# Kernel optimization log

Measured on AMD Instinct MI355X. Metric: run time of the kernel, lower is better.

Reference implementation:

```python
import jax, jax.numpy as jnp
import numpy as np

B = 65536          # batch of response rows
R = 262144         # number of response rows
N_CELLS = 900
N_MISSING = 100
N_DRUGS = 256
NFEAT = 1024
CELL_EMB = 1024
DRUG_EMB = 128
HID = 200
NDOSES = 9


def setup_inputs() -> dict:
    key = jax.random.key(0)
    ks = jax.random.split(key, 16)
    inp = {
        "idx": jax.random.randint(ks[0], (B,), 0, R, dtype=jnp.int32),
        "tidx": jax.random.randint(ks[1], (B,), 0, R, dtype=jnp.int32),
        "is_missing": jax.random.randint(ks[2], (R,), 0, 2, dtype=jnp.int32),
        "cell_map": jax.random.randint(ks[3], (R,), 0, N_MISSING, dtype=jnp.int32),
        "drug_map": jax.random.randint(ks[4], (R,), 0, N_DRUGS, dtype=jnp.int32),
        "cell_features": jax.random.normal(ks[5], (N_CELLS, NFEAT), jnp.float32),
        "missing_emb": jax.random.normal(ks[6], (N_MISSING, CELL_EMB), jnp.float32) * 0.02,
        "drug_emb": jax.random.normal(ks[7], (N_DRUGS, DRUG_EMB), jnp.float32) * 0.02,
        "W1": jax.random.normal(ks[8], (NFEAT, CELL_EMB), jnp.float32) * 0.02,
        "b1": jax.random.normal(ks[9], (CELL_EMB,), jnp.float32) * 0.02,
        "Wf1": jax.random.normal(ks[10], (CELL_EMB + DRUG_EMB, HID), jnp.float32) * 0.02,
        "bf1": jax.random.normal(ks[11], (HID,), jnp.float32) * 0.02,
        "Wf2": jax.random.normal(ks[12], (HID, HID), jnp.float32) * 0.02,
        "bf2": jax.random.normal(ks[13], (HID,), jnp.float32) * 0.02,
        "Wf3": jax.random.normal(ks[14], (HID, NDOSES), jnp.float32) * 0.02,
        "bf3": jax.random.normal(ks[15], (NDOSES,), jnp.float32) * 0.02,
    }
    return inp


def _l2_normalize(x, eps=1e-12):
    # torch F.normalize: x / max(||x||_2, eps)
    n = jnp.sqrt(jnp.sum(x * x, axis=1, keepdims=True))
    return x / jnp.maximum(n, eps)


def reference(idx, tidx, is_missing, cell_map, drug_map, cell_features,
              missing_emb, drug_emb, W1, b1, Wf1, bf1, Wf2, bf2, Wf3, bf3):
    # --- cell_lookup, vectorized (eval mode: dropout = identity) ---
    cm = cell_map[idx]                                   # [B]
    miss = (is_missing[idx] != 0)[:, None]               # [B,1] bool
    feat = cell_features[cm]                             # [B, NFEAT]
    present = jax.nn.relu(feat @ W1 + b1)                # [B, CELL_EMB]
    missing = missing_emb[cm]                            # [B, CELL_EMB]
    cell_embeds = jnp.where(miss, missing, present)
    # --- drug_lookup ---
    drug_embeds = drug_emb[drug_map[tidx]]               # [B, DRUG_EMB]
    # --- embeds_to_predictions ---
    cell_embeds = _l2_normalize(cell_embeds)
    drug_embeds = _l2_normalize(drug_embeds)
    x = jnp.concatenate([cell_embeds, drug_embeds], axis=1)
    h = jax.nn.relu(x @ Wf1 + bf1)
    h = jax.nn.relu(h @ Wf2 + bf2)
    fwd = h @ Wf3 + bf3                                  # [B, NDOSES]
    base = fwd[:, 0:1]
    mu = jnp.concatenate(
        [base, base + jnp.cumsum(jax.nn.softplus(fwd[:, 1:]), axis=1)], axis=1)
    return mu  # [B, NDOSES + ... ] -> actually [B, 1 + (NDOSES-1) + 1]? No: [B, NDOSES]? see note
```

## Files before the change

kernel.cpp:

```cpp
#include <hip/hip_runtime.h>
#include <hip/hip_bf16.h>

#define NFEAT 1024
#define CELL_EMB 1024
#define DRUG_EMB 128
#define HID 200
#define NDOSES 9
#define N_MISSING 100
#define N_DRUGS 256
#define S 16
#define MUSTRIDE 12

typedef __hip_bfloat16 bf16;
typedef __attribute__((ext_vector_type(8))) short short8;
typedef __attribute__((ext_vector_type(4))) short short4v;
typedef __attribute__((ext_vector_type(4))) float float4v;

__device__ __forceinline__ float bf2f(short s) {
    unsigned u = ((unsigned)(unsigned short)s) << 16;
    return __builtin_bit_cast(float, u);
}
__device__ __forceinline__ short f2bf(float f) {
    unsigned u = __builtin_bit_cast(unsigned, f);
    unsigned r = (u + 0x7FFFu + ((u >> 16) & 1u)) >> 16;
    return (short)r;
}
template <bool F32>
__device__ __forceinline__ float ld(const void* p, int i) {
    if (F32) return ((const float*)p)[i];
    return bf2f(((const short*)p)[i]);
}
__device__ __forceinline__ float ldr(const void* p, int i, bool f32) {
    return f32 ? ((const float*)p)[i] : bf2f(((const short*)p)[i]);
}
__device__ __forceinline__ float softplusf(float x) {
    return (x > 20.f) ? x : log1pf(expf(x));
}

__device__ __forceinline__ bool sniff_f32(const unsigned short* __restrict__ w1) {
    int lane = threadIdx.x & 63;
    unsigned short h = w1[lane];
    bool hit = ((lane & 1) == 0) && (((h >> 7) & 0xFFu) >= 130u);
    return __ballot(hit) != 0ull;
}


#define GP_PRESENT 800
#define GP_DC_END (GP_PRESENT + 256)
#define GP_PB_END (GP_DC_END + 25)
#define GP_CZ_END (GP_PB_END + 40)

__global__ __launch_bounds__(256) void mega_prep_k(const void* __restrict__ CF,
                                                   const unsigned short* __restrict__ W1u,
                                                   const void* __restrict__ b1,
                                                   const void* __restrict__ drug_emb,
                                                   const void* __restrict__ Wf1,
                                                   const void* __restrict__ Wf2,
                                                   float* __restrict__ P8,
                                                   float* __restrict__ Dc,
                                                   short8* __restrict__ Bf,
                                                   float* __restrict__ Cc) {
    bool f32 = sniff_f32(W1u);
    const void* W1 = (const void*)W1u;
    int blk = blockIdx.x, tid = threadIdx.x;

    if (blk < GP_PRESENT) {
        __shared__ float feat[128];
        int c = blk >> 3, kc = blk & 7;
        if (tid < 128) feat[tid] = ldr(CF, c * NFEAT + kc * 128 + tid, f32);
        __syncthreads();
        int j0 = tid * 4;
        float a0 = 0.f, a1 = 0.f, a2 = 0.f, a3 = 0.f;
        if (f32) {
            const float* w = (const float*)W1 + (size_t)(kc * 128) * CELL_EMB + j0;
#pragma unroll 8
            for (int k = 0; k < 128; ++k) {
                float4v wv = *(const float4v*)(w + (size_t)k * CELL_EMB);
                float fk = feat[k];
                a0 = fmaf(fk, wv[0], a0); a1 = fmaf(fk, wv[1], a1);
                a2 = fmaf(fk, wv[2], a2); a3 = fmaf(fk, wv[3], a3);
            }
        } else {
            const short* w = (const short*)W1 + (size_t)(kc * 128) * CELL_EMB + j0;
#pragma unroll 8
            for (int k = 0; k < 128; ++k) {
                short4v wv = *(const short4v*)(w + (size_t)k * CELL_EMB);
                float fk = feat[k];
                a0 = fmaf(fk, bf2f(wv[0]), a0); a1 = fmaf(fk, bf2f(wv[1]), a1);
                a2 = fmaf(fk, bf2f(wv[2]), a2); a3 = fmaf(fk, bf2f(wv[3]), a3);
            }
        }
        if (kc == 0) {
            a0 += ldr(b1, j0 + 0, f32); a1 += ldr(b1, j0 + 1, f32);
            a2 += ldr(b1, j0 + 2, f32); a3 += ldr(b1, j0 + 3, f32);
        }
        float4v o; o[0] = a0; o[1] = a1; o[2] = a2; o[3] = a3;
        *(float4v*)(P8 + ((size_t)(kc * N_MISSING + c)) * CELL_EMB + j0) = o;
    } else if (blk < GP_DC_END) {
        __shared__ float x[DRUG_EMB];
        __shared__ float red[4];
        int d = blk - GP_PRESENT;
        if (tid < DRUG_EMB) x[tid] = ldr(drug_emb, d * DRUG_EMB + tid, f32);
        __syncthreads();
        float ss = 0.f;
        if (tid < DRUG_EMB) ss = x[tid] * x[tid];
        for (int o = 32; o > 0; o >>= 1) ss += __shfl_down(ss, o, 64);
        if ((tid & 63) == 0) red[tid >> 6] = ss;
        __syncthreads();
        float inv = 1.f / fmaxf(sqrtf(red[0] + red[1] + red[2] + red[3]), 1e-12f);
        if (tid < HID) {
            float acc = 0.f;
#pragma unroll 8
            for (int k = 0; k < DRUG_EMB; ++k)
                acc = fmaf(x[k], ldr(Wf1, (CELL_EMB + k) * HID + tid, f32), acc);
            Dc[d * HID + tid] = acc * inv;
        }
    } else if (blk < GP_PB_END) {
        int t = (blk - GP_DC_END) * 256 + tid;
        if (t < 6272) {
            int l = t & 63, chunk = t >> 6;
            int p = chunk / 49, rem = chunk - p * 49;
            int nt = rem / 7, s = rem - nt * 7;
            int n = p * 112 + nt * 16 + (l & 15);
            int k0 = s * 32 + (l >> 4) * 8;
            short8 v;
#pragma unroll
            for (int j = 0; j < 8; ++j) {
                int k = k0 + j;
                v[j] = (k < HID && n < HID) ? f2bf(ldr(Wf2, k * HID + n, f32)) : (short)0;
            }
            Bf[t] = v;
        }
    } else {
        int i = (blk - GP_PB_END) * 1024 + tid * 4;
        if (i < 200 * HID) {
            float4v z; z[0] = 0.f; z[1] = 0.f; z[2] = 0.f; z[3] = 0.f;
            *(float4v*)(Cc + i) = z;
        }
    }
}

__global__ __launch_bounds__(256) void cc_k(const unsigned short* __restrict__ W1u,
                                            const float* __restrict__ P8,
                                            const void* __restrict__ missing_emb,
                                            const void* __restrict__ Wf1,
                                            float* __restrict__ Cc) {
    __shared__ __align__(16) float x[128];
    __shared__ float red[4];
    bool f32 = sniff_f32(W1u);
    int r = blockIdx.x, kc = blockIdx.y, tid = threadIdx.x;
    int e0 = tid * 4;
    float4v v;
    if (r < N_MISSING) {
        v[0] = 0.f; v[1] = 0.f; v[2] = 0.f; v[3] = 0.f;
#pragma unroll
        for (int p = 0; p < 8; ++p) {
            float4v t = *(const float4v*)(P8 + ((size_t)(p * N_MISSING + r)) * CELL_EMB + e0);
            v[0] += t[0]; v[1] += t[1]; v[2] += t[2]; v[3] += t[3];
        }
        v[0] = fmaxf(v[0], 0.f); v[1] = fmaxf(v[1], 0.f);
        v[2] = fmaxf(v[2], 0.f); v[3] = fmaxf(v[3], 0.f);
    } else if (f32) {
        v = *(const float4v*)((const float*)missing_emb + (size_t)(r - N_MISSING) * CELL_EMB + e0);
    } else {
        short4v s = *(const short4v*)((const short*)missing_emb + (size_t)(r - N_MISSING) * CELL_EMB + e0);
        v[0] = bf2f(s[0]); v[1] = bf2f(s[1]); v[2] = bf2f(s[2]); v[3] = bf2f(s[3]);
    }
    if ((tid >> 5) == kc) *(float4v*)(x + (e0 - kc * 128)) = v;
    float ss = v[0] * v[0] + v[1] * v[1] + v[2] * v[2] + v[3] * v[3];
    for (int o = 32; o > 0; o >>= 1) ss += __shfl_down(ss, o, 64);
    if ((tid & 63) == 0) red[tid >> 6] = ss;
    __syncthreads();
    float inv = 1.f / fmaxf(sqrtf(red[0] + red[1] + red[2] + red[3]), 1e-12f);
    if (tid < HID) {
        float acc = 0.f;
        if (f32) {
            const float* w = (const float*)Wf1 + (size_t)(kc * 128) * HID + tid;
#pragma unroll 8
            for (int k = 0; k < 128; ++k)
                acc = fmaf(x[k], w[(size_t)k * HID], acc);
        } else {
            const short* w = (const short*)Wf1 + (size_t)(kc * 128) * HID + tid;
#pragma unroll 8
            for (int k = 0; k < 128; ++k)
                acc = fmaf(x[k], bf2f(w[(size_t)k * HID]), acc);
        }
        atomicAdd(&Cc[r * HID + tid], acc * inv);
    }
}

#define KSTEPS 7
#define NTP 7
#define KP 224
#define MB 64

__global__ __launch_bounds__(256) void pair_k(const unsigned short* __restrict__ W1u,
                                              const float* __restrict__ Cc,
                                              const float* __restrict__ Dc,
                                              const void* __restrict__ bf1,
                                              const void* __restrict__ bf2,
                                              const void* __restrict__ Wf3,
                                              const short8* __restrict__ Bf,
                                              float* __restrict__ mu) {
    __shared__ float Crow[KP];
    __shared__ float bf2s[KP];
    __shared__ short wf3s[KP * NDOSES];
    bool f32 = sniff_f32(W1u);
    int tid = threadIdx.x;
    int lane = tid & 63, w = tid >> 6;
    int q = lane >> 4, col = lane & 15;
    int r0 = blockIdx.x * MB;
    int c = r0 >> 8;
    int d0 = r0 & 255;

    for (int k = tid; k < KP; k += 256) {
        Crow[k] = (k < HID) ? Cc[c * HID + k] + ldr(bf1, k, f32) : 0.f;
        bf2s[k] = (k < HID) ? ldr(bf2, k, f32) : 0.f;
    }
    for (int t = tid; t < KP * NDOSES; t += 256) {
        int k = t / NDOSES, dd = t - k * NDOSES;
        wf3s[t] = (k < HID) ? f2bf(ldr(Wf3, k * NDOSES + dd, f32)) : (short)0;
    }
    __syncthreads();

    int arow = d0 + w * 16 + col;

    short8 a[KSTEPS];
#pragma unroll
    for (int s = 0; s < KSTEPS; ++s) {
        int k0 = s * 32 + q * 8;
        if (k0 < HID) {
            float4v c0 = *(const float4v*)(&Crow[k0]);
            float4v c1 = *(const float4v*)(&Crow[k0 + 4]);
            float4v dv0 = *(const float4v*)(Dc + (size_t)arow * HID + k0);
            float4v dv1 = *(const float4v*)(Dc + (size_t)arow * HID + k0 + 4);
#pragma unroll
            for (int j = 0; j < 4; ++j) {
                a[s][j]     = f2bf(fmaxf(c0[j] + dv0[j], 0.f));
                a[s][j + 4] = f2bf(fmaxf(c1[j] + dv1[j], 0.f));
            }
        } else {
#pragma unroll
            for (int j = 0; j < 8; ++j) a[s][j] = 0;
        }
    }

    float fw[4][9];
#pragma unroll
    for (int i = 0; i < 4; ++i)
#pragma unroll
        for (int dd = 0; dd < 9; ++dd) fw[i][dd] = 0.f;

    for (int p = 0; p < 2; ++p) {
        float4v acc[NTP];
#pragma unroll
        for (int nt = 0; nt < NTP; ++nt) acc[nt] = 0.f;
#pragma unroll
        for (int s = 0; s < KSTEPS; ++s) {
#pragma unroll
            for (int nt = 0; nt < NTP; ++nt) {
                short8 bb = Bf[(size_t)((p * 7 + nt) * 7 + s) * 64 + lane];
                acc[nt] = __builtin_amdgcn_mfma_f32_16x16x32_bf16(a[s], bb, acc[nt], 0, 0, 0);
            }
        }
#pragma unroll
        for (int nt = 0; nt < NTP; ++nt) {
            int n = p * 112 + nt * 16 + col;
            float bb2 = bf2s[n];
            float w3[9];
#pragma unroll
            for (int dd = 0; dd < 9; ++dd) w3[dd] = bf2f(wf3s[n * NDOSES + dd]);
#pragma unroll
            for (int rg = 0; rg < 4; ++rg) {
                float h2 = fmaxf(acc[nt][rg] + bb2, 0.f);
#pragma unroll
                for (int dd = 0; dd < 9; ++dd)
                    fw[rg][dd] = fmaf(h2, w3[dd], fw[rg][dd]);
            }
        }
    }
#pragma unroll
    for (int i = 0; i < 4; ++i)
#pragma unroll
        for (int dd = 0; dd < 9; ++dd) {
            float v = fw[i][dd];
            v += __shfl_xor(v, 1, 16);
            v += __shfl_xor(v, 2, 16);
            v += __shfl_xor(v, 4, 16);
            v += __shfl_xor(v, 8, 16);
            fw[i][dd] = v;
        }
#pragma unroll
    for (int i = 0; i < 4; ++i) {
        int row = r0 + w * 16 + q * 4 + i;
        float myval = 0.f;
#pragma unroll
        for (int dd = 0; dd < 9; ++dd) myval = (col == dd) ? fw[i][dd] : myval;
        float v = (col == 0) ? myval : softplusf(myval);
        float t1 = __shfl_up(v, 1, 16); if (col >= 1) v += t1;
        float t2 = __shfl_up(v, 2, 16); if (col >= 2) v += t2;
        float t4 = __shfl_up(v, 4, 16); if (col >= 4) v += t4;
        float t8 = __shfl_up(v, 8, 16); if (col >= 8) v += t8;
        if (col < NDOSES) mu[(size_t)row * MUSTRIDE + col] = v;
    }
}

__global__ __launch_bounds__(256) void gather_k(const unsigned short* __restrict__ W1u,
                                                const int* __restrict__ idx,
                                                const int* __restrict__ tidx,
                                                const int* __restrict__ is_missing,
                                                const int* __restrict__ cell_map,
                                                const int* __restrict__ drug_map,
                                                const float* __restrict__ mu,
                                                void* __restrict__ out, int nB) {
    bool f32 = sniff_f32(W1u);
    int b = blockIdx.x * 256 + threadIdx.x;
    if (b >= nB) return;
    int i = idx[b];
    int cm = cell_map[i];
    int kc = (is_missing[i] != 0) ? (N_MISSING + cm) : cm;
    int kd = drug_map[tidx[b]];
    const float* mr = mu + (size_t)(kc * 256 + kd) * MUSTRIDE;
    float4v m0 = *(const float4v*)mr;
    float4v m1 = *(const float4v*)(mr + 4);
    float m8 = mr[8];
    float vals[9] = {m0[0], m0[1], m0[2], m0[3], m1[0], m1[1], m1[2], m1[3], m8};
    if (f32) {
        float* o = (float*)out + (size_t)b * NDOSES;
#pragma unroll
        for (int dd = 0; dd < 9; ++dd) o[dd] = vals[dd];
    } else {
        short* o = (short*)out + (size_t)b * NDOSES;
#pragma unroll
        for (int dd = 0; dd < 9; ++dd) o[dd] = f2bf(vals[dd]);
    }
}


__global__ void sniff_kernel(const unsigned short* __restrict__ w1bits, int* __restrict__ flag) {
    if (threadIdx.x == 0 && blockIdx.x == 0) {
        int f = 0;
        for (int i = 0; i < 512; ++i) {
            unsigned int e = (w1bits[i] >> 7) & 0xFFu;
            if (e >= 130u) f = 1;
        }
        *flag = f;
    }
}

template <bool F32>
__global__ __launch_bounds__(256) void present_kernel(const int* __restrict__ flag,
                                                      const void* __restrict__ cell_features,
                                                      const void* __restrict__ W1,
                                                      const void* __restrict__ b1,
                                                      float* __restrict__ P) {
    if (*flag != (int)F32) return;
    __shared__ float feat[NFEAT];
    int c = blockIdx.x, jb = blockIdx.y;
    for (int k = threadIdx.x; k < NFEAT; k += 256)
        feat[k] = ld<F32>(cell_features, c * NFEAT + k);
    __syncthreads();
    int j = jb * 256 + threadIdx.x;
    float acc = ld<F32>(b1, j);
    for (int k = 0; k < NFEAT; ++k)
        acc = fmaf(feat[k], ld<F32>(W1, k * CELL_EMB + j), acc);
    P[c * CELL_EMB + j] = fmaxf(acc, 0.f);
}

template <bool F32>
__global__ __launch_bounds__(256) void cc_kernel(const int* __restrict__ flag,
                                                 const float* __restrict__ P,
                                                 const void* __restrict__ missing_emb,
                                                 const void* __restrict__ Wf1,
                                                 float* __restrict__ Cc) {
    if (*flag != (int)F32) return;
    int r = blockIdx.x;
    __shared__ float x[CELL_EMB];
    __shared__ float red[4];
    if (r < N_MISSING) {
        for (int k = threadIdx.x; k < CELL_EMB; k += 256) x[k] = P[r * CELL_EMB + k];
    } else {
        for (int k = threadIdx.x; k < CELL_EMB; k += 256)
            x[k] = ld<F32>(missing_emb, (r - N_MISSING) * CELL_EMB + k);
    }
    __syncthreads();
    float ss = 0.f;
    for (int k = threadIdx.x; k < CELL_EMB; k += 256) ss += x[k] * x[k];
    for (int o = 32; o > 0; o >>= 1) ss += __shfl_down(ss, o, 64);
    if ((threadIdx.x & 63) == 0) red[threadIdx.x >> 6] = ss;
    __syncthreads();
    float inv = 1.f / fmaxf(sqrtf(red[0] + red[1] + red[2] + red[3]), 1e-12f);
    int j = threadIdx.x;
    if (j < HID) {
        float acc = 0.f;
        for (int k = 0; k < CELL_EMB; ++k)
            acc = fmaf(x[k], ld<F32>(Wf1, k * HID + j), acc);
        Cc[r * HID + j] = acc * inv;
    }
}

template <bool F32>
__global__ __launch_bounds__(256) void dc_kernel(const int* __restrict__ flag,
                                                 const void* __restrict__ drug_emb,
                                                 const void* __restrict__ Wf1,
                                                 float* __restrict__ Dc) {
    if (*flag != (int)F32) return;
    int d = blockIdx.x;
    __shared__ float x[DRUG_EMB];
    __shared__ float red[4];
    if (threadIdx.x < DRUG_EMB) x[threadIdx.x] = ld<F32>(drug_emb, d * DRUG_EMB + threadIdx.x);
    __syncthreads();
    float ss = 0.f;
    if (threadIdx.x < DRUG_EMB) ss = x[threadIdx.x] * x[threadIdx.x];
    for (int o = 32; o > 0; o >>= 1) ss += __shfl_down(ss, o, 64);
    if ((threadIdx.x & 63) == 0) red[threadIdx.x >> 6] = ss;
    __syncthreads();
    float inv = 1.f / fmaxf(sqrtf(red[0] + red[1] + red[2] + red[3]), 1e-12f);
    int j = threadIdx.x;
    if (j < HID) {
        float acc = 0.f;
        for (int k = 0; k < DRUG_EMB; ++k)
            acc = fmaf(x[k], ld<F32>(Wf1, (CELL_EMB + k) * HID + j), acc);
        Dc[d * HID + j] = acc * inv;
    }
}

template <bool F32>
__global__ __launch_bounds__(256) void main_kernel(const int* __restrict__ flag,
                                                   const int* __restrict__ idx,
                                                   const int* __restrict__ tidx,
                                                   const int* __restrict__ is_missing,
                                                   const int* __restrict__ cell_map,
                                                   const int* __restrict__ drug_map,
                                                   const float* __restrict__ Cc,
                                                   const float* __restrict__ Dc,
                                                   const void* __restrict__ bf1,
                                                   const void* __restrict__ Wf2,
                                                   const void* __restrict__ bf2,
                                                   const void* __restrict__ Wf3,
                                                   const void* __restrict__ bf3,
                                                   void* __restrict__ out, int nB) {
    if (*flag != (int)F32) return;
    __shared__ float h1t[HID][S];
    __shared__ float h2[S][HID];
    __shared__ float wf3s[HID * NDOSES];
    __shared__ float bf3s[NDOSES];
    __shared__ int keyc[S], keyd[S];
    __shared__ float fwds[S][NDOSES];

    int b0 = blockIdx.x * S;
    int tid = threadIdx.x;

    if (tid < S) {
        int b = b0 + tid;
        if (b < nB) {
            int i = idx[b];
            int cm = cell_map[i];
            keyc[tid] = (is_missing[i] != 0) ? (N_MISSING + cm) : cm;
            keyd[tid] = drug_map[tidx[b]];
        } else { keyc[tid] = 0; keyd[tid] = 0; }
    }
    for (int t = tid; t < HID * NDOSES; t += 256) wf3s[t] = ld<F32>(Wf3, t);
    if (tid < NDOSES) bf3s[tid] = ld<F32>(bf3, tid);
    __syncthreads();

    for (int t = tid; t < S * HID; t += 256) {
        int s = t / HID;
        int j = t - s * HID;
        float v = Cc[keyc[s] * HID + j] + Dc[keyd[s] * HID + j] + ld<F32>(bf1, j);
        h1t[j][s] = fmaxf(v, 0.f);
    }
    __syncthreads();

    if (tid < HID) {
        float acc[S];
#pragma unroll
        for (int s = 0; s < S; ++s) acc[s] = 0.f;
        for (int i = 0; i < HID; ++i) {
            float wv = ld<F32>(Wf2, i * HID + tid);
#pragma unroll
            for (int s = 0; s < S; ++s) acc[s] = fmaf(h1t[i][s], wv, acc[s]);
        }
        float bb = ld<F32>(bf2, tid);
#pragma unroll
        for (int s = 0; s < S; ++s) h2[s][tid] = fmaxf(acc[s] + bb, 0.f);
    }
    __syncthreads();

    if (tid < S * NDOSES) {
        int s = tid / NDOSES;
        int k = tid - s * NDOSES;
        float acc = bf3s[k];
        for (int j = 0; j < HID; ++j)
            acc = fmaf(h2[s][j], wf3s[j * NDOSES + k], acc);
        fwds[s][k] = acc;
    }
    __syncthreads();

    if (tid < S && b0 + tid < nB) {
        float m = fwds[tid][0];
        long o = (long)(b0 + tid) * NDOSES;
        if (F32) ((float*)out)[o] = m; else ((short*)out)[o] = f2bf(m);
#pragma unroll
        for (int k = 1; k < NDOSES; ++k) {
            float x = fwds[tid][k];
            m += softplusf(x);
            if (F32) ((float*)out)[o + k] = m;
            else     ((short*)out)[o + k] = f2bf(m);
        }
    }
}


extern "C" void kernel_launch(void* const* d_in, const int* in_sizes, int n_in,
                              void* d_out, int out_size, void* d_ws, size_t ws_size,
                              hipStream_t stream) {
    const int* idx        = (const int*)d_in[0];
    const int* tidx       = (const int*)d_in[1];
    const int* is_missing = (const int*)d_in[2];
    const int* cell_map   = (const int*)d_in[3];
    const int* drug_map   = (const int*)d_in[4];
    const void* CF   = d_in[5];
    const void* memb = d_in[6];
    const void* demb = d_in[7];
    const void* W1   = d_in[8];
    const void* b1   = d_in[9];
    const void* Wf1  = d_in[10];
    const void* bf1v = d_in[11];
    const void* Wf2  = d_in[12];
    const void* bf2v = d_in[13];
    const void* Wf3  = d_in[14];
    const void* bf3v = d_in[15];

    int nB = in_sizes[0];
    const size_t NEED = 935552ull * 4ull;

    if (ws_size >= NEED) {
        float* ws   = (float*)d_ws;
        float* Cc   = ws + 64;
        float* Dc   = ws + 40064;
        float* Bf   = ws + 91264;
        float* P8   = ws + 116352;
        float* mu   = P8;

        hipLaunchKernelGGL(mega_prep_k, dim3(GP_CZ_END), dim3(256), 0, stream,
                           CF, (const unsigned short*)W1, b1, demb, Wf1, Wf2,
                           P8, Dc, (short8*)Bf, Cc);
        hipLaunchKernelGGL(cc_k, dim3(2 * N_MISSING, 8), dim3(256), 0, stream,
                           (const unsigned short*)W1, P8, memb, Wf1, Cc);
        hipLaunchKernelGGL(pair_k, dim3(800), dim3(256), 0, stream,
                           (const unsigned short*)W1, Cc, Dc, bf1v, bf2v, Wf3,
                           (const short8*)Bf, mu);
        hipLaunchKernelGGL(gather_k, dim3((nB + 255) / 256), dim3(256), 0, stream,
                           (const unsigned short*)W1, idx, tidx, is_missing,
                           cell_map, drug_map, mu, d_out, nB);
    } else {
        float* ws   = (float*)d_ws;
        int*   flag = (int*)d_ws;
        float* P    = ws + 64;
        float* Cc   = P + 102400;
        float* Dc   = Cc + 40000;

        hipLaunchKernelGGL(sniff_kernel, dim3(1), dim3(64), 0, stream,
                           (const unsigned short*)W1, flag);
#define LAUNCH_BOTH(name, grid, blk, ...)                                          \
        hipLaunchKernelGGL((name<false>), grid, blk, 0, stream, flag, __VA_ARGS__);\
        hipLaunchKernelGGL((name<true>),  grid, blk, 0, stream, flag, __VA_ARGS__);
        LAUNCH_BOTH(present_kernel, dim3(N_MISSING, 4), dim3(256), CF, W1, b1, P)
        LAUNCH_BOTH(cc_kernel, dim3(2 * N_MISSING), dim3(256), P, memb, Wf1, Cc)
        LAUNCH_BOTH(dc_kernel, dim3(N_DRUGS), dim3(256), demb, Wf1, Dc)
        LAUNCH_BOTH(main_kernel, dim3((nB + S - 1) / S), dim3(256),
                    idx, tidx, is_missing, cell_map, drug_map, Cc, Dc,
                    bf1v, Wf2, bf2v, Wf3, bf3v, d_out, nB)
#undef LAUNCH_BOTH
    }
}
```

Baseline: 162.1 us.

## Fuse cell-embedding first-layer projection into pair kernel, drop cc_k launch

Removes the separate cc_k kernel and the Cc zeroing pass. Each pair_k block now rebuilds its cell row (sum of partial present products plus relu, or the missing embedding), L2-normalises it and computes the full 1024-long projection through Wf1 itself. This saves one launch, the atomics and a round trip through global memory. In exchange, each of the 800 blocks does a serial 1024-step dot product per thread before its main work, and mu is moved to a separate workspace region because it no longer aliases P8.

```diff
diff --git a/kernel.cpp b/kernel.cpp
--- a/kernel.cpp
+++ b/kernel.cpp
@@ -48,7 +48,6 @@
 #define GP_PRESENT 800
 #define GP_DC_END (GP_PRESENT + 256)
 #define GP_PB_END (GP_DC_END + 25)
-#define GP_CZ_END (GP_PB_END + 40)
 
 __global__ __launch_bounds__(256) void mega_prep_k(const void* __restrict__ CF,
                                                    const unsigned short* __restrict__ W1u,
@@ -58,8 +57,7 @@
                                                    const void* __restrict__ Wf2,
                                                    float* __restrict__ P8,
                                                    float* __restrict__ Dc,
-                                                   short8* __restrict__ Bf,
-                                                   float* __restrict__ Cc) {
+                                                   short8* __restrict__ Bf) {
     bool f32 = sniff_f32(W1u);
     const void* W1 = (const void*)W1u;
     int blk = blockIdx.x, tid = threadIdx.x;
@@ -115,7 +113,7 @@
                 acc = fmaf(x[k], ldr(Wf1, (CELL_EMB + k) * HID + tid, f32), acc);
             Dc[d * HID + tid] = acc * inv;
         }
-    } else if (blk < GP_PB_END) {
+    } else {
         int t = (blk - GP_DC_END) * 256 + tid;
         if (t < 6272) {
             int l = t & 63, chunk = t >> 6;
@@ -131,61 +129,6 @@
             }
             Bf[t] = v;
         }
-    } else {
-        int i = (blk - GP_PB_END) * 1024 + tid * 4;
-        if (i < 200 * HID) {
-            float4v z; z[0] = 0.f; z[1] = 0.f; z[2] = 0.f; z[3] = 0.f;
-            *(float4v*)(Cc + i) = z;
-        }
-    }
-}
-
-__global__ __launch_bounds__(256) void cc_k(const unsigned short* __restrict__ W1u,
-                                            const float* __restrict__ P8,
-                                            const void* __restrict__ missing_emb,
-                                            const void* __restrict__ Wf1,
-                                            float* __restrict__ Cc) {
-    __shared__ __align__(16) float x[128];
-    __shared__ float red[4];
-    bool f32 = sniff_f32(W1u);
-    int r = blockIdx.x, kc = blockIdx.y, tid = threadIdx.x;
-    int e0 = tid * 4;
-    float4v v;
-    if (r < N_MISSING) {
-        v[0] = 0.f; v[1] = 0.f; v[2] = 0.f; v[3] = 0.f;
-#pragma unroll
-        for (int p = 0; p < 8; ++p) {
-            float4v t = *(const float4v*)(P8 + ((size_t)(p * N_MISSING + r)) * CELL_EMB + e0);
-            v[0] += t[0]; v[1] += t[1]; v[2] += t[2]; v[3] += t[3];
-        }
-        v[0] = fmaxf(v[0], 0.f); v[1] = fmaxf(v[1], 0.f);
-        v[2] = fmaxf(v[2], 0.f); v[3] = fmaxf(v[3], 0.f);
-    } else if (f32) {
-        v = *(const float4v*)((const float*)missing_emb + (size_t)(r - N_MISSING) * CELL_EMB + e0);
-    } else {
-        short4v s = *(const short4v*)((const short*)missing_emb + (size_t)(r - N_MISSING) * CELL_EMB + e0);
-        v[0] = bf2f(s[0]); v[1] = bf2f(s[1]); v[2] = bf2f(s[2]); v[3] = bf2f(s[3]);
-    }
-    if ((tid >> 5) == kc) *(float4v*)(x + (e0 - kc * 128)) = v;
-    float ss = v[0] * v[0] + v[1] * v[1] + v[2] * v[2] + v[3] * v[3];
-    for (int o = 32; o > 0; o >>= 1) ss += __shfl_down(ss, o, 64);
-    if ((tid & 63) == 0) red[tid >> 6] = ss;
-    __syncthreads();
-    float inv = 1.f / fmaxf(sqrtf(red[0] + red[1] + red[2] + red[3]), 1e-12f);
-    if (tid < HID) {
-        float acc = 0.f;
-        if (f32) {
-            const float* w = (const float*)Wf1 + (size_t)(kc * 128) * HID + tid;
-#pragma unroll 8
-            for (int k = 0; k < 128; ++k)
-                acc = fmaf(x[k], w[(size_t)k * HID], acc);
-        } else {
-            const short* w = (const short*)Wf1 + (size_t)(kc * 128) * HID + tid;
-#pragma unroll 8
-            for (int k = 0; k < 128; ++k)
-                acc = fmaf(x[k], bf2f(w[(size_t)k * HID]), acc);
-        }
-        atomicAdd(&Cc[r * HID + tid], acc * inv);
     }
 }
 
@@ -195,13 +138,17 @@
 #define MB 64
 
 __global__ __launch_bounds__(256) void pair_k(const unsigned short* __restrict__ W1u,
-                                              const float* __restrict__ Cc,
+                                              const float* __restrict__ P8,
+                                              const void* __restrict__ missing_emb,
+                                              const void* __restrict__ Wf1,
                                               const float* __restrict__ Dc,
                                               const void* __restrict__ bf1,
                                               const void* __restrict__ bf2,
                                               const void* __restrict__ Wf3,
                                               const short8* __restrict__ Bf,
                                               float* __restrict__ mu) {
+    __shared__ __align__(16) float x[CELL_EMB];
+    __shared__ float red[4];
     __shared__ float Crow[KP];
     __shared__ float bf2s[KP];
     __shared__ short wf3s[KP * NDOSES];
@@ -213,9 +160,48 @@
     int c = r0 >> 8;
     int d0 = r0 & 255;
 
-    for (int k = tid; k < KP; k += 256) {
-        Crow[k] = (k < HID) ? Cc[c * HID + k] + ldr(bf1, k, f32) : 0.f;
-        bf2s[k] = (k < HID) ? ldr(bf2, k, f32) : 0.f;
+    int e0 = tid * 4;
+    float4v v;
+    if (c < N_MISSING) {
+        v[0] = 0.f; v[1] = 0.f; v[2] = 0.f; v[3] = 0.f;
+#pragma unroll
+        for (int p = 0; p < 8; ++p) {
+            float4v t = *(const float4v*)(P8 + ((size_t)(p * N_MISSING + c)) * CELL_EMB + e0);
+            v[0] += t[0]; v[1] += t[1]; v[2] += t[2]; v[3] += t[3];
+        }
+        v[0] = fmaxf(v[0], 0.f); v[1] = fmaxf(v[1], 0.f);
+        v[2] = fmaxf(v[2], 0.f); v[3] = fmaxf(v[3], 0.f);
+    } else if (f32) {
+        v = *(const float4v*)((const float*)missing_emb + (size_t)(c - N_MISSING) * CELL_EMB + e0);
+    } else {
+        short4v s = *(const short4v*)((const short*)missing_emb + (size_t)(c - N_MISSING) * CELL_EMB + e0);
+        v[0] = bf2f(s[0]); v[1] = bf2f(s[1]); v[2] = bf2f(s[2]); v[3] = bf2f(s[3]);
+    }
+    *(float4v*)(x + e0) = v;
+    float ss = v[0] * v[0] + v[1] * v[1] + v[2] * v[2] + v[3] * v[3];
+    for (int o = 32; o > 0; o >>= 1) ss += __shfl_down(ss, o, 64);
+    if ((tid & 63) == 0) red[tid >> 6] = ss;
+    __syncthreads();
+    float inv = 1.f / fmaxf(sqrtf(red[0] + red[1] + red[2] + red[3]), 1e-12f);
+
+    if (tid < HID) {
+        float acc = 0.f;
+        if (f32) {
+            const float* wp = (const float*)Wf1 + tid;
+#pragma unroll 8
+            for (int k = 0; k < CELL_EMB; ++k)
+                acc = fmaf(x[k], wp[(size_t)k * HID], acc);
+        } else {
+            const short* wp = (const short*)Wf1 + tid;
+#pragma unroll 8
+            for (int k = 0; k < CELL_EMB; ++k)
+                acc = fmaf(x[k], bf2f(wp[(size_t)k * HID]), acc);
+        }
+        Crow[tid] = acc * inv + ldr(bf1, tid, f32);
+    }
+    if (tid < KP) {
+        if (tid >= HID) Crow[tid] = 0.f;
+        bf2s[tid] = (tid < HID) ? ldr(bf2, tid, f32) : 0.f;
     }
     for (int t = tid; t < KP * NDOSES; t += 256) {
         int k = t / NDOSES, dd = t - k * NDOSES;
@@ -283,12 +269,12 @@
     for (int i = 0; i < 4; ++i)
 #pragma unroll
         for (int dd = 0; dd < 9; ++dd) {
-            float v = fw[i][dd];
-            v += __shfl_xor(v, 1, 16);
-            v += __shfl_xor(v, 2, 16);
-            v += __shfl_xor(v, 4, 16);
-            v += __shfl_xor(v, 8, 16);
-            fw[i][dd] = v;
+            float vv = fw[i][dd];
+            vv += __shfl_xor(vv, 1, 16);
+            vv += __shfl_xor(vv, 2, 16);
+            vv += __shfl_xor(vv, 4, 16);
+            vv += __shfl_xor(vv, 8, 16);
+            fw[i][dd] = vv;
         }
 #pragma unroll
     for (int i = 0; i < 4; ++i) {
@@ -296,12 +282,12 @@
         float myval = 0.f;
 #pragma unroll
         for (int dd = 0; dd < 9; ++dd) myval = (col == dd) ? fw[i][dd] : myval;
-        float v = (col == 0) ? myval : softplusf(myval);
-        float t1 = __shfl_up(v, 1, 16); if (col >= 1) v += t1;
-        float t2 = __shfl_up(v, 2, 16); if (col >= 2) v += t2;
-        float t4 = __shfl_up(v, 4, 16); if (col >= 4) v += t4;
-        float t8 = __shfl_up(v, 8, 16); if (col >= 8) v += t8;
-        if (col < NDOSES) mu[(size_t)row * MUSTRIDE + col] = v;
+        float vv = (col == 0) ? myval : softplusf(myval);
+        float t1 = __shfl_up(vv, 1, 16); if (col >= 1) vv += t1;
+        float t2 = __shfl_up(vv, 2, 16); if (col >= 2) vv += t2;
+        float t4 = __shfl_up(vv, 4, 16); if (col >= 4) vv += t4;
+        float t8 = __shfl_up(vv, 8, 16); if (col >= 8) vv += t8;
+        if (col < NDOSES) mu[(size_t)row * MUSTRIDE + col] = vv;
     }
 }
 
@@ -533,24 +519,21 @@
     const void* bf3v = d_in[15];
 
     int nB = in_sizes[0];
-    const size_t NEED = 935552ull * 4ull;
+    const size_t NEED = 1509952ull * 4ull;
 
     if (ws_size >= NEED) {
         float* ws   = (float*)d_ws;
-        float* Cc   = ws + 64;
-        float* Dc   = ws + 40064;
-        float* Bf   = ws + 91264;
-        float* P8   = ws + 116352;
-        float* mu   = P8;
-
-        hipLaunchKernelGGL(mega_prep_k, dim3(GP_CZ_END), dim3(256), 0, stream,
+        float* Dc   = ws + 64;
+        float* Bf   = ws + 51264;
+        float* P8   = ws + 76352;
+        float* mu   = ws + 895552;
+
+        hipLaunchKernelGGL(mega_prep_k, dim3(GP_PB_END), dim3(256), 0, stream,
                            CF, (const unsigned short*)W1, b1, demb, Wf1, Wf2,
-                           P8, Dc, (short8*)Bf, Cc);
-        hipLaunchKernelGGL(cc_k, dim3(2 * N_MISSING, 8), dim3(256), 0, stream,
-                           (const unsigned short*)W1, P8, memb, Wf1, Cc);
+                           P8, Dc, (short8*)Bf);
         hipLaunchKernelGGL(pair_k, dim3(800), dim3(256), 0, stream,
-                           (const unsigned short*)W1, Cc, Dc, bf1v, bf2v, Wf3,
-                           (const short8*)Bf, mu);
+                           (const unsigned short*)W1, P8, memb, Wf1, Dc,
+                           bf1v, bf2v, Wf3, (const short8*)Bf, mu);
         hipLaunchKernelGGL(gather_k, dim3((nB + 255) / 256), dim3(256), 0, stream,
                            (const unsigned short*)W1, idx, tidx, is_missing,
                            cell_map, drug_map, mu, d_out, nB);
```

Result: slower. 229.9 us (+41.8%).
